# Performance work log

Hardware: AMD Instinct MI355X
Metric: run time of the kernel (lower is better)

Reference implementation:

```python
import jax, jax.numpy as jnp
import numpy as np

N_NODES = 50000


def sage_conv(x, src, dst, Wl, bl, Wr):
    # PyG SAGEConv (aggr='mean'): out = lin_l(mean_j x_j) + lin_r(x_i)
    msg = x[src]                                            # [E, d] gather
    agg = jax.ops.segment_sum(msg, dst, num_segments=N_NODES)   # [N, d]
    cnt = jax.ops.segment_sum(jnp.ones_like(dst, dtype=x.dtype), dst,
                              num_segments=N_NODES)         # [N]
    agg = agg / jnp.maximum(cnt, 1.0)[:, None]
    return agg @ Wl.T + bl + x @ Wr.T


def setup_inputs() -> dict:
    key = jax.random.key(0)
    ks = jax.random.split(key, 8)
    d = 64
    x = jax.random.normal(ks[0], (N_NODES, d), dtype=jnp.float32)
    edge_index = jax.random.randint(ks[1], (2, 800000), 0, N_NODES, dtype=jnp.int64)
    s = 1.0 / np.sqrt(d)
    Wl0 = jax.random.uniform(ks[2], (d, d), jnp.float32, -s, s)
    bl0 = jax.random.uniform(ks[3], (d,), jnp.float32, -s, s)
    Wr0 = jax.random.uniform(ks[4], (d, d), jnp.float32, -s, s)
    Wl1 = jax.random.uniform(ks[5], (d, d), jnp.float32, -s, s)
    bl1 = jax.random.uniform(ks[6], (d,), jnp.float32, -s, s)
    Wr1 = jax.random.uniform(ks[7], (d, d), jnp.float32, -s, s)
    return {"x": x, "edge_index": edge_index,
            "Wl0": Wl0, "bl0": bl0, "Wr0": Wr0,
            "Wl1": Wl1, "bl1": bl1, "Wr1": Wr1}


def reference(x, edge_index, Wl0, bl0, Wr0, Wl1, bl1, Wr1):
    src, dst = edge_index[0], edge_index[1]
    h = sage_conv(x, src, dst, Wl0, bl0, Wr0)
    h = jax.nn.relu(h)
    h = sage_conv(h, src, dst, Wl1, bl1, Wr1)
    return h
```

## Files before the change

### kernel.cpp

```cpp
#include <hip/hip_runtime.h>

#define N_NODES 50000
#define D 64
#define BKT_SHIFT 10
#define BKT_NODES 1024
#define NBKT ((N_NODES + BKT_NODES - 1) / BKT_NODES)
#define CAP 18432
#define GPAD 32
#define XBLOCKS ((N_NODES * D / 4) / 256)

typedef __attribute__((ext_vector_type(4))) float f4;
typedef __attribute__((ext_vector_type(4))) unsigned uv4;
typedef __attribute__((ext_vector_type(4))) unsigned short us4;
typedef __attribute__((ext_vector_type(8))) short bf16x8;
typedef __attribute__((ext_vector_type(4))) float f32x4;

static __device__ __forceinline__ unsigned short f2bf(float f) {
    unsigned u = __builtin_bit_cast(unsigned, f);
    unsigned r = (u + 0x7fffu + ((u >> 16) & 1u)) >> 16;
    return (unsigned short)r;
}
static __device__ __forceinline__ float bflo(unsigned w) {
    return __builtin_bit_cast(float, w << 16);
}
static __device__ __forceinline__ float bfhi(unsigned w) {
    return __builtin_bit_cast(float, w & 0xffff0000u);
}

static __device__ __forceinline__ int detect_is64(const unsigned* __restrict__ ei32) {
    int lane = threadIdx.x & 63;
    unsigned v = (lane < 32) ? ei32[2 * lane + 1] : 0u;
    return (__ballot(v != 0u) == 0ull) ? 1 : 0;
}

static __device__ __forceinline__ int load_edges4(const unsigned* __restrict__ ei32,
                                                  int is64, int E, int base,
                                                  int* s, int* d) {
    if (base + 3 < E) {
        if (is64) {
            uv4 sa = *(const uv4*)&ei32[2 * base];
            uv4 sb = *(const uv4*)&ei32[2 * base + 4];
            uv4 da = *(const uv4*)&ei32[2 * (E + base)];
            uv4 db = *(const uv4*)&ei32[2 * (E + base) + 4];
            s[0] = (int)sa[0]; s[1] = (int)sa[2]; s[2] = (int)sb[0]; s[3] = (int)sb[2];
            d[0] = (int)da[0]; d[1] = (int)da[2]; d[2] = (int)db[0]; d[3] = (int)db[2];
        } else {
            uv4 sa = *(const uv4*)&ei32[base];
            uv4 da = *(const uv4*)&ei32[E + base];
            s[0] = (int)sa[0]; s[1] = (int)sa[1]; s[2] = (int)sa[2]; s[3] = (int)sa[3];
            d[0] = (int)da[0]; d[1] = (int)da[1]; d[2] = (int)da[2]; d[3] = (int)da[3];
        }
        return 4;
    }
    int c = 0;
    for (int e = base; e < E && e < base + 4; ++e, ++c) {
        s[c] = is64 ? (int)ei32[2 * e] : (int)ei32[e];
        d[c] = is64 ? (int)ei32[2 * (E + e)] : (int)ei32[E + e];
    }
    return c;
}

__global__ __launch_bounds__(256) void cvt_all(const float* __restrict__ x,
                                               unsigned short* __restrict__ xb,
                                               const float* __restrict__ Wl0,
                                               const float* __restrict__ Wr0,
                                               const float* __restrict__ Wl1,
                                               const float* __restrict__ Wr1,
                                               unsigned short* __restrict__ Wlb0,
                                               unsigned short* __restrict__ Wrb0,
                                               unsigned short* __restrict__ Wlb1,
                                               unsigned short* __restrict__ Wrb1,
                                               int* __restrict__ gcur) {
    int b = blockIdx.x, tid = threadIdx.x;
    if (b < XBLOCKS) {
        int i = (b * 256 + tid) * 4;
        f4 v = *(const f4*)&x[i];
        us4 o;
        o[0] = f2bf(v[0]); o[1] = f2bf(v[1]); o[2] = f2bf(v[2]); o[3] = f2bf(v[3]);
        *(us4*)&xb[i] = o;
    } else if (b < XBLOCKS + 4) {
        int w = b - XBLOCKS;
        const float* src = (w == 0) ? Wl0 : (w == 1) ? Wr0 : (w == 2) ? Wl1 : Wr1;
        unsigned short* dst = (w == 0) ? Wlb0 : (w == 1) ? Wrb0 : (w == 2) ? Wlb1 : Wrb1;
        for (int i = tid * 4; i < 64 * 64; i += 1024) {
            f4 v = *(const f4*)&src[i];
            us4 o;
            o[0] = f2bf(v[0]); o[1] = f2bf(v[1]); o[2] = f2bf(v[2]); o[3] = f2bf(v[3]);
            *(us4*)&dst[i] = o;
        }
    } else {
        if (tid < NBKT) gcur[tid * GPAD] = tid * CAP;
    }
}

__global__ __launch_bounds__(256) void bin_kernel(const unsigned* __restrict__ ei32,
                                                  int E, int* __restrict__ gcur,
                                                  unsigned* __restrict__ binned) {
    __shared__ int bc[NBKT];
    __shared__ int boff[NBKT];
    int tid = threadIdx.x;
    if (tid < NBKT) bc[tid] = 0;
    __syncthreads();
    int is64 = detect_is64(ei32);
    int base = (blockIdx.x * 256 + tid) * 8;
    int s[8], d[8];
    int c = 0;
    if (base < E) {
        c = load_edges4(ei32, is64, E, base, s, d);
        if (base + 4 < E) c += load_edges4(ei32, is64, E, base + 4, s + 4, d + 4);
    }
    for (int t = 0; t < c; ++t) atomicAdd(&bc[d[t] >> BKT_SHIFT], 1);
    __syncthreads();
    if (tid < NBKT) {
        int v = bc[tid];
        boff[tid] = v ? atomicAdd(&gcur[tid * GPAD], v) : 0;
        bc[tid] = 0;
    }
    __syncthreads();
    for (int t = 0; t < c; ++t) {
        int bkt = d[t] >> BKT_SHIFT;
        int pos = boff[bkt] + atomicAdd(&bc[bkt], 1);
        if (pos < (bkt + 1) * CAP)
            binned[pos] = ((unsigned)(d[t] & (BKT_NODES - 1)) << 16) | (unsigned)s[t];
    }
}

__global__ __launch_bounds__(1024) void build_kernel(const unsigned* __restrict__ binned,
                                                     const int* __restrict__ gcur,
                                                     int2* __restrict__ rp2,
                                                     unsigned short* __restrict__ ssrc, int n) {
    __shared__ int nc[BKT_NODES];
    __shared__ int wpart[16];
    int b = blockIdx.x;
    int tid = threadIdx.x;
    int ebase = b * CAP;
    int eend = gcur[b * GPAD];
    if (eend > ebase + CAP) eend = ebase + CAP;
    nc[tid] = 0;
    __syncthreads();
    for (int i = ebase + tid; i < eend; i += 1024)
        atomicAdd(&nc[binned[i] >> 16], 1);
    __syncthreads();
    int v = nc[tid];
    int lane = tid & 63, wv = tid >> 6;
    int incl = v;
#pragma unroll
    for (int off = 1; off < 64; off <<= 1) {
        int t = __shfl_up(incl, off);
        if (lane >= off) incl += t;
    }
    if (lane == 63) wpart[wv] = incl;
    __syncthreads();
    int pre = 0;
    for (int w2 = 0; w2 < wv; ++w2) pre += wpart[w2];
    int run = ebase + pre + incl - v;
    int node = b * BKT_NODES + tid;
    nc[tid] = run;
    if (node < n) rp2[node] = make_int2(run, v);
    __syncthreads();
    for (int i = ebase + tid; i < eend; i += 1024) {
        unsigned u = binned[i];
        int pos = atomicAdd(&nc[u >> 16], 1);
        ssrc[pos] = (unsigned short)(u & 0xffffu);
    }
}

template <bool RELU, bool LAST>
__global__ __launch_bounds__(256) void sage_fused(const unsigned short* __restrict__ xb,
                                                  const int2* __restrict__ rp2,
                                                  const unsigned short* __restrict__ ssrc,
                                                  const unsigned short* __restrict__ Wlb,
                                                  const float* __restrict__ bl,
                                                  const unsigned short* __restrict__ Wrb,
                                                  float* __restrict__ out,
                                                  unsigned short* __restrict__ ob, int n) {
    __shared__ f4 lred[4][4][64];
    int tid = threadIdx.x;
    int wv = tid >> 6;
    int lane = tid & 63;
    int nb = blockIdx.x * 16;
    int row = lane & 15;
    int half = lane >> 4;
    int koff = half * 8;
    int node = nb + row;
    int2 bd = rp2[node];
    int deg = bd.y;
    int chunk = (deg + 3) >> 2;
    int beg = bd.x + wv * chunk;
    int end = bd.x + deg;
    if (end > beg + chunk) end = beg + chunk;

    f4 acc4[4];
#pragma unroll
    for (int q = 0; q < 4; ++q) acc4[q] = (f4){0.f, 0.f, 0.f, 0.f};

    int e = beg;
    for (; e + 1 < end; e += 2) {
        int s0 = ssrc[e], s1 = ssrc[e + 1];
        uv4 v0 = *(const uv4*)(xb + (size_t)s0 * 64 + koff);
        uv4 v1 = *(const uv4*)(xb + (size_t)s0 * 64 + 32 + koff);
        uv4 v2 = *(const uv4*)(xb + (size_t)s1 * 64 + koff);
        uv4 v3 = *(const uv4*)(xb + (size_t)s1 * 64 + 32 + koff);
#pragma unroll
        for (int q = 0; q < 2; ++q) {
            acc4[q][0] += bflo(v0[2 * q])     + bflo(v2[2 * q]);
            acc4[q][1] += bfhi(v0[2 * q])     + bfhi(v2[2 * q]);
            acc4[q][2] += bflo(v0[2 * q + 1]) + bflo(v2[2 * q + 1]);
            acc4[q][3] += bfhi(v0[2 * q + 1]) + bfhi(v2[2 * q + 1]);
            acc4[2 + q][0] += bflo(v1[2 * q])     + bflo(v3[2 * q]);
            acc4[2 + q][1] += bfhi(v1[2 * q])     + bfhi(v3[2 * q]);
            acc4[2 + q][2] += bflo(v1[2 * q + 1]) + bflo(v3[2 * q + 1]);
            acc4[2 + q][3] += bfhi(v1[2 * q + 1]) + bfhi(v3[2 * q + 1]);
        }
    }
    if (e < end) {
        int s0 = ssrc[e];
        uv4 v0 = *(const uv4*)(xb + (size_t)s0 * 64 + koff);
        uv4 v1 = *(const uv4*)(xb + (size_t)s0 * 64 + 32 + koff);
#pragma unroll
        for (int q = 0; q < 2; ++q) {
            acc4[q][0] += bflo(v0[2 * q]);
            acc4[q][1] += bfhi(v0[2 * q]);
            acc4[q][2] += bflo(v0[2 * q + 1]);
            acc4[q][3] += bfhi(v0[2 * q + 1]);
            acc4[2 + q][0] += bflo(v1[2 * q]);
            acc4[2 + q][1] += bfhi(v1[2 * q]);
            acc4[2 + q][2] += bflo(v1[2 * q + 1]);
            acc4[2 + q][3] += bfhi(v1[2 * q + 1]);
        }
    }

#pragma unroll
    for (int q = 0; q < 4; ++q) lred[q][wv][lane] = acc4[q];
    __syncthreads();
#pragma unroll
    for (int w2 = 0; w2 < 4; ++w2) {
        if (w2 == wv) continue;
#pragma unroll
        for (int q = 0; q < 4; ++q) acc4[q] += lred[q][w2][lane];
    }

    float inv = 1.0f / (float)(deg > 1 ? deg : 1);
    uv4 pa0, pa1;
#pragma unroll
    for (int q = 0; q < 2; ++q) {
        pa0[2 * q]     = (unsigned)f2bf(acc4[q][0] * inv) |
                         ((unsigned)f2bf(acc4[q][1] * inv) << 16);
        pa0[2 * q + 1] = (unsigned)f2bf(acc4[q][2] * inv) |
                         ((unsigned)f2bf(acc4[q][3] * inv) << 16);
        pa1[2 * q]     = (unsigned)f2bf(acc4[2 + q][0] * inv) |
                         ((unsigned)f2bf(acc4[2 + q][1] * inv) << 16);
        pa1[2 * q + 1] = (unsigned)f2bf(acc4[2 + q][2] * inv) |
                         ((unsigned)f2bf(acc4[2 + q][3] * inv) << 16);
    }
    bf16x8 a0 = __builtin_bit_cast(bf16x8, pa0);
    bf16x8 a1 = __builtin_bit_cast(bf16x8, pa1);
    bf16x8 x0 = *(const bf16x8*)&xb[(size_t)node * 64 + koff];
    bf16x8 x1 = *(const bf16x8*)&xb[(size_t)node * 64 + 32 + koff];

    int o = wv * 16 + row;
    float bv = bl[o];
    f32x4 accd = (f32x4){bv, bv, bv, bv};
    bf16x8 wl0 = *(const bf16x8*)&Wlb[(size_t)o * 64 + koff];
    bf16x8 wl1 = *(const bf16x8*)&Wlb[(size_t)o * 64 + 32 + koff];
    bf16x8 wr0 = *(const bf16x8*)&Wrb[(size_t)o * 64 + koff];
    bf16x8 wr1 = *(const bf16x8*)&Wrb[(size_t)o * 64 + 32 + koff];
    accd = __builtin_amdgcn_mfma_f32_16x16x32_bf16(a0, wl0, accd, 0, 0, 0);
    accd = __builtin_amdgcn_mfma_f32_16x16x32_bf16(a1, wl1, accd, 0, 0, 0);
    accd = __builtin_amdgcn_mfma_f32_16x16x32_bf16(x0, wr0, accd, 0, 0, 0);
    accd = __builtin_amdgcn_mfma_f32_16x16x32_bf16(x1, wr1, accd, 0, 0, 0);

#pragma unroll
    for (int r = 0; r < 4; ++r) {
        float v = accd[r];
        if (RELU) v = fmaxf(v, 0.f);
        int nd = nb + half * 4 + r;
        if (LAST) out[(size_t)nd * 64 + o] = v;
        else      ob[(size_t)nd * 64 + o] = f2bf(v);
    }
}

extern "C" void kernel_launch(void* const* d_in, const int* in_sizes, int n_in,
                              void* d_out, int out_size, void* d_ws, size_t ws_size,
                              hipStream_t stream) {
    const float* x      = (const float*)d_in[0];
    const unsigned* ei  = (const unsigned*)d_in[1];
    const float* Wl0    = (const float*)d_in[2];
    const float* bl0    = (const float*)d_in[3];
    const float* Wr0    = (const float*)d_in[4];
    const float* Wl1    = (const float*)d_in[5];
    const float* bl1    = (const float*)d_in[6];
    const float* Wr1    = (const float*)d_in[7];
    float* out          = (float*)d_out;

    const int N = N_NODES;
    const int E = in_sizes[1] / 2;

    char* w = (char*)d_ws;
    auto take = [&](size_t bytes) {
        char* p = w;
        w += (bytes + 255) & ~(size_t)255;
        return p;
    };
    int*            gcur   = (int*)take((size_t)NBKT * GPAD * sizeof(int));
    unsigned*       binned = (unsigned*)take((size_t)NBKT * CAP * sizeof(unsigned));
    int2*           rp2    = (int2*)take((size_t)N * sizeof(int2));
    unsigned short* ssrc   = (unsigned short*)take((size_t)NBKT * CAP * sizeof(unsigned short));
    unsigned short* xb     = (unsigned short*)take((size_t)N * D * sizeof(unsigned short));
    unsigned short* hb     = (unsigned short*)take((size_t)N * D * sizeof(unsigned short));
    unsigned short* Wlb0   = (unsigned short*)take((size_t)D * D * sizeof(unsigned short));
    unsigned short* Wrb0   = (unsigned short*)take((size_t)D * D * sizeof(unsigned short));
    unsigned short* Wlb1   = (unsigned short*)take((size_t)D * D * sizeof(unsigned short));
    unsigned short* Wrb1   = (unsigned short*)take((size_t)D * D * sizeof(unsigned short));

    cvt_all<<<XBLOCKS + 5, 256, 0, stream>>>(x, xb, Wl0, Wr0, Wl1, Wr1,
                                             Wlb0, Wrb0, Wlb1, Wrb1, gcur);
    int edgeBlocks = (E + 2047) / 2048;
    bin_kernel<<<edgeBlocks, 256, 0, stream>>>(ei, E, gcur, binned);
    build_kernel<<<NBKT, 1024, 0, stream>>>(binned, gcur, rp2, ssrc, N);

    int fusedBlocks = (N + 15) / 16;
    sage_fused<true, false><<<fusedBlocks, 256, 0, stream>>>(xb, rp2, ssrc, Wlb0, bl0, Wrb0,
                                                             nullptr, hb, N);
    sage_fused<false, true><<<fusedBlocks, 256, 0, stream>>>(hb, rp2, ssrc, Wlb1, bl1, Wrb1,
                                                             out, nullptr, N);
}
```

Measured before the change: 164.5 us.

## Merge conversion and edge binning into one kernel, unroll gather by four

Result: slower. 169.6 us (+3.1%).

```diff
diff --git a/kernel.cpp b/kernel.cpp
--- a/kernel.cpp
+++ b/kernel.cpp
@@ -60,17 +60,21 @@
     return c;
 }
 
-__global__ __launch_bounds__(256) void cvt_all(const float* __restrict__ x,
-                                               unsigned short* __restrict__ xb,
-                                               const float* __restrict__ Wl0,
-                                               const float* __restrict__ Wr0,
-                                               const float* __restrict__ Wl1,
-                                               const float* __restrict__ Wr1,
-                                               unsigned short* __restrict__ Wlb0,
-                                               unsigned short* __restrict__ Wrb0,
-                                               unsigned short* __restrict__ Wlb1,
-                                               unsigned short* __restrict__ Wrb1,
-                                               int* __restrict__ gcur) {
+__global__ __launch_bounds__(256) void setup_kernel(const float* __restrict__ x,
+                                                    unsigned short* __restrict__ xb,
+                                                    const float* __restrict__ Wl0,
+                                                    const float* __restrict__ Wr0,
+                                                    const float* __restrict__ Wl1,
+                                                    const float* __restrict__ Wr1,
+                                                    unsigned short* __restrict__ Wlb0,
+                                                    unsigned short* __restrict__ Wrb0,
+                                                    unsigned short* __restrict__ Wlb1,
+                                                    unsigned short* __restrict__ Wrb1,
+                                                    const unsigned* __restrict__ ei32,
+                                                    int E, int* __restrict__ gcur,
+                                                    unsigned* __restrict__ binned) {
+    __shared__ int bc[NBKT];
+    __shared__ int boff[NBKT];
     int b = blockIdx.x, tid = threadIdx.x;
     if (b < XBLOCKS) {
         int i = (b * 256 + tid) * 4;
@@ -78,7 +82,9 @@
         us4 o;
         o[0] = f2bf(v[0]); o[1] = f2bf(v[1]); o[2] = f2bf(v[2]); o[3] = f2bf(v[3]);
         *(us4*)&xb[i] = o;
-    } else if (b < XBLOCKS + 4) {
+        return;
+    }
+    if (b < XBLOCKS + 4) {
         int w = b - XBLOCKS;
         const float* src = (w == 0) ? Wl0 : (w == 1) ? Wr0 : (w == 2) ? Wl1 : Wr1;
         unsigned short* dst = (w == 0) ? Wlb0 : (w == 1) ? Wrb0 : (w == 2) ? Wlb1 : Wrb1;
@@ -88,21 +94,13 @@
             o[0] = f2bf(v[0]); o[1] = f2bf(v[1]); o[2] = f2bf(v[2]); o[3] = f2bf(v[3]);
             *(us4*)&dst[i] = o;
         }
-    } else {
-        if (tid < NBKT) gcur[tid * GPAD] = tid * CAP;
-    }
-}
-
-__global__ __launch_bounds__(256) void bin_kernel(const unsigned* __restrict__ ei32,
-                                                  int E, int* __restrict__ gcur,
-                                                  unsigned* __restrict__ binned) {
-    __shared__ int bc[NBKT];
-    __shared__ int boff[NBKT];
-    int tid = threadIdx.x;
+        return;
+    }
+    int bb = b - (XBLOCKS + 4);
     if (tid < NBKT) bc[tid] = 0;
     __syncthreads();
     int is64 = detect_is64(ei32);
-    int base = (blockIdx.x * 256 + tid) * 8;
+    int base = (bb * 256 + tid) * 8;
     int s[8], d[8];
     int c = 0;
     if (base < E) {
@@ -113,7 +111,7 @@
     __syncthreads();
     if (tid < NBKT) {
         int v = bc[tid];
-        boff[tid] = v ? atomicAdd(&gcur[tid * GPAD], v) : 0;
+        boff[tid] = v ? (tid * CAP + atomicAdd(&gcur[tid * GPAD], v)) : 0;
         bc[tid] = 0;
     }
     __syncthreads();
@@ -134,8 +132,9 @@
     int b = blockIdx.x;
     int tid = threadIdx.x;
     int ebase = b * CAP;
-    int eend = gcur[b * GPAD];
-    if (eend > ebase + CAP) eend = ebase + CAP;
+    int cnt = gcur[b * GPAD];
+    if (cnt > CAP) cnt = CAP;
+    int eend = ebase + cnt;
     nc[tid] = 0;
     __syncthreads();
     for (int i = ebase + tid; i < eend; i += 1024)
@@ -190,43 +189,56 @@
     int end = bd.x + deg;
     if (end > beg + chunk) end = beg + chunk;
 
+    bf16x8 x0 = *(const bf16x8*)&xb[(size_t)node * 64 + koff];
+    bf16x8 x1 = *(const bf16x8*)&xb[(size_t)node * 64 + 32 + koff];
+    int o = wv * 16 + row;
+    bf16x8 wl0 = *(const bf16x8*)&Wlb[(size_t)o * 64 + koff];
+    bf16x8 wl1 = *(const bf16x8*)&Wlb[(size_t)o * 64 + 32 + koff];
+    bf16x8 wr0 = *(const bf16x8*)&Wrb[(size_t)o * 64 + koff];
+    bf16x8 wr1 = *(const bf16x8*)&Wrb[(size_t)o * 64 + 32 + koff];
+    float bv = bl[o];
+
     f4 acc4[4];
 #pragma unroll
     for (int q = 0; q < 4; ++q) acc4[q] = (f4){0.f, 0.f, 0.f, 0.f};
 
     int e = beg;
-    for (; e + 1 < end; e += 2) {
-        int s0 = ssrc[e], s1 = ssrc[e + 1];
-        uv4 v0 = *(const uv4*)(xb + (size_t)s0 * 64 + koff);
-        uv4 v1 = *(const uv4*)(xb + (size_t)s0 * 64 + 32 + koff);
-        uv4 v2 = *(const uv4*)(xb + (size_t)s1 * 64 + koff);
-        uv4 v3 = *(const uv4*)(xb + (size_t)s1 * 64 + 32 + koff);
+    for (; e + 3 < end; e += 4) {
+        int s0 = ssrc[e], s1 = ssrc[e + 1], s2 = ssrc[e + 2], s3 = ssrc[e + 3];
+        uv4 r0 = *(const uv4*)(xb + (size_t)s0 * 64 + koff);
+        uv4 r1 = *(const uv4*)(xb + (size_t)s0 * 64 + 32 + koff);
+        uv4 r2 = *(const uv4*)(xb + (size_t)s1 * 64 + koff);
+        uv4 r3 = *(const uv4*)(xb + (size_t)s1 * 64 + 32 + koff);
+        uv4 r4 = *(const uv4*)(xb + (size_t)s2 * 64 + koff);
+        uv4 r5 = *(const uv4*)(xb + (size_t)s2 * 64 + 32 + koff);
+        uv4 r6 = *(const uv4*)(xb + (size_t)s3 * 64 + koff);
+        uv4 r7 = *(const uv4*)(xb + (size_t)s3 * 64 + 32 + koff);
 #pragma unroll
         for (int q = 0; q < 2; ++q) {
-            acc4[q][0] += bflo(v0[2 * q])     + bflo(v2[2 * q]);
-            acc4[q][1] += bfhi(v0[2 * q])     + bfhi(v2[2 * q]);
-            acc4[q][2] += bflo(v0[2 * q + 1]) + bflo(v2[2 * q + 1]);
-            acc4[q][3] += bfhi(v0[2 * q + 1]) + bfhi(v2[2 * q + 1]);
-            acc4[2 + q][0] += bflo(v1[2 * q])     + bflo(v3[2 * q]);
-            acc4[2 + q][1] += bfhi(v1[2 * q])     + bfhi(v3[2 * q]);
-            acc4[2 + q][2] += bflo(v1[2 * q + 1]) + bflo(v3[2 * q + 1]);
-            acc4[2 + q][3] += bfhi(v1[2 * q + 1]) + bfhi(v3[2 * q + 1]);
+            acc4[q][0] += (bflo(r0[2 * q]) + bflo(r2[2 * q])) + (bflo(r4[2 * q]) + bflo(r6[2 * q]));
+            acc4[q][1] += (bfhi(r0[2 * q]) + bfhi(r2[2 * q])) + (bfhi(r4[2 * q]) + bfhi(r6[2 * q]));
+            acc4[q][2] += (bflo(r0[2 * q + 1]) + bflo(r2[2 * q + 1])) + (bflo(r4[2 * q + 1]) + bflo(r6[2 * q + 1]));
+            acc4[q][3] += (bfhi(r0[2 * q + 1]) + bfhi(r2[2 * q + 1])) + (bfhi(r4[2 * q + 1]) + bfhi(r6[2 * q + 1]));
+            acc4[2 + q][0] += (bflo(r1[2 * q]) + bflo(r3[2 * q])) + (bflo(r5[2 * q]) + bflo(r7[2 * q]));
+            acc4[2 + q][1] += (bfhi(r1[2 * q]) + bfhi(r3[2 * q])) + (bfhi(r5[2 * q]) + bfhi(r7[2 * q]));
+            acc4[2 + q][2] += (bflo(r1[2 * q + 1]) + bflo(r3[2 * q + 1])) + (bflo(r5[2 * q + 1]) + bflo(r7[2 * q + 1]));
+            acc4[2 + q][3] += (bfhi(r1[2 * q + 1]) + bfhi(r3[2 * q + 1])) + (bfhi(r5[2 * q + 1]) + bfhi(r7[2 * q + 1]));
         }
     }
-    if (e < end) {
+    for (; e < end; ++e) {
         int s0 = ssrc[e];
-        uv4 v0 = *(const uv4*)(xb + (size_t)s0 * 64 + koff);
-        uv4 v1 = *(const uv4*)(xb + (size_t)s0 * 64 + 32 + koff);
+        uv4 r0 = *(const uv4*)(xb + (size_t)s0 * 64 + koff);
+        uv4 r1 = *(const uv4*)(xb + (size_t)s0 * 64 + 32 + koff);
 #pragma unroll
         for (int q = 0; q < 2; ++q) {
-            acc4[q][0] += bflo(v0[2 * q]);
-            acc4[q][1] += bfhi(v0[2 * q]);
-            acc4[q][2] += bflo(v0[2 * q + 1]);
-            acc4[q][3] += bfhi(v0[2 * q + 1]);
-            acc4[2 + q][0] += bflo(v1[2 * q]);
-            acc4[2 + q][1] += bfhi(v1[2 * q]);
-            acc4[2 + q][2] += bflo(v1[2 * q + 1]);
-            acc4[2 + q][3] += bfhi(v1[2 * q + 1]);
+            acc4[q][0] += bflo(r0[2 * q]);
+            acc4[q][1] += bfhi(r0[2 * q]);
+            acc4[q][2] += bflo(r0[2 * q + 1]);
+            acc4[q][3] += bfhi(r0[2 * q + 1]);
+            acc4[2 + q][0] += bflo(r1[2 * q]);
+            acc4[2 + q][1] += bfhi(r1[2 * q]);
+            acc4[2 + q][2] += bflo(r1[2 * q + 1]);
+            acc4[2 + q][3] += bfhi(r1[2 * q + 1]);
         }
     }
 
@@ -255,16 +267,8 @@
     }
     bf16x8 a0 = __builtin_bit_cast(bf16x8, pa0);
     bf16x8 a1 = __builtin_bit_cast(bf16x8, pa1);
-    bf16x8 x0 = *(const bf16x8*)&xb[(size_t)node * 64 + koff];
-    bf16x8 x1 = *(const bf16x8*)&xb[(size_t)node * 64 + 32 + koff];
-
-    int o = wv * 16 + row;
-    float bv = bl[o];
+
     f32x4 accd = (f32x4){bv, bv, bv, bv};
-    bf16x8 wl0 = *(const bf16x8*)&Wlb[(size_t)o * 64 + koff];
-    bf16x8 wl1 = *(const bf16x8*)&Wlb[(size_t)o * 64 + 32 + koff];
-    bf16x8 wr0 = *(const bf16x8*)&Wrb[(size_t)o * 64 + koff];
-    bf16x8 wr1 = *(const bf16x8*)&Wrb[(size_t)o * 64 + 32 + koff];
     accd = __builtin_amdgcn_mfma_f32_16x16x32_bf16(a0, wl0, accd, 0, 0, 0);
     accd = __builtin_amdgcn_mfma_f32_16x16x32_bf16(a1, wl1, accd, 0, 0, 0);
     accd = __builtin_amdgcn_mfma_f32_16x16x32_bf16(x0, wr0, accd, 0, 0, 0);
@@ -313,10 +317,10 @@
     unsigned short* Wlb1   = (unsigned short*)take((size_t)D * D * sizeof(unsigned short));
     unsigned short* Wrb1   = (unsigned short*)take((size_t)D * D * sizeof(unsigned short));
 
-    cvt_all<<<XBLOCKS + 5, 256, 0, stream>>>(x, xb, Wl0, Wr0, Wl1, Wr1,
-                                             Wlb0, Wrb0, Wlb1, Wrb1, gcur);
+    hipMemsetAsync(gcur, 0, (size_t)NBKT * GPAD * sizeof(int), stream);
     int edgeBlocks = (E + 2047) / 2048;
-    bin_kernel<<<edgeBlocks, 256, 0, stream>>>(ei, E, gcur, binned);
+    setup_kernel<<<XBLOCKS + 4 + edgeBlocks, 256, 0, stream>>>(
+        x, xb, Wl0, Wr0, Wl1, Wr1, Wlb0, Wrb0, Wlb1, Wrb1, ei, E, gcur, binned);
     build_kernel<<<NBKT, 1024, 0, stream>>>(binned, gcur, rp2, ssrc, N);
 
     int fusedBlocks = (N + 15) / 16;
```
